# Performance work log

Hardware: AMD Instinct MI355X
Metric: run time of the kernel (lower is better)

The kernel has to match this reference:

```python
import math
import jax, jax.numpy as jnp
import numpy as np

HEAD = 16
DIM = 1024
DH = DIM // HEAD
NEG = -100000000.0


def setup_inputs() -> dict:
    key = jax.random.key(0)
    ks = jax.random.split(key, 12)
    B, S, D = 2, 2048, DIM
    s = 1.0 / math.sqrt(D)
    return {
        "key": jax.random.normal(ks[0], (B, S, D), jnp.float32),
        "value": jax.random.normal(ks[1], (B, S, D), jnp.float32),
        "query": jax.random.normal(ks[2], (B, S, D), jnp.float32),
        "mask": jax.random.randint(ks[3], (B, 1, S, S), 0, 2) == 1,
        "Wq": jax.random.normal(ks[4], (D, D), jnp.float32) * s,
        "bq": jnp.zeros((D,), jnp.float32),
        "Wk": jax.random.normal(ks[5], (D, D), jnp.float32) * s,
        "bk": jnp.zeros((D,), jnp.float32),
        "Wv": jax.random.normal(ks[6], (D, D), jnp.float32) * s,
        "bv": jnp.zeros((D,), jnp.float32),
        "Wo": jax.random.normal(ks[7], (D, D), jnp.float32) * s,
        "bo": jnp.zeros((D,), jnp.float32),
    }


def _split_heads(x, b):
    # [B, S, D] -> [B, H, S, Dh]
    return x.reshape(b, -1, HEAD, DH).transpose(0, 2, 1, 3)


def reference(key, value, query, mask, Wq, bq, Wk, bk, Wv, bv, Wo, bo):
    b, k_len, d = key.shape
    q_len = query.shape[1]
    k_up = _split_heads(key @ Wk.T + bk, b)
    v_up = _split_heads(value @ Wv.T + bv, b)
    q_up = _split_heads(query @ Wq.T + bq, b) / math.sqrt(DH)
    scores = jnp.einsum("bhqd,bhkd->bhqk", q_up, k_up)
    scores = jnp.where(mask, NEG, scores)
    attn = jax.nn.softmax(scores, axis=-1)
    # dropout is identity in eval/reference mode
    context = jnp.einsum("bhqk,bhkd->bhqd", attn, v_up)
    context = context.transpose(0, 2, 1, 3).reshape(b, q_len, d)
    out = context @ Wo.T + bo
    return out, attn
```

## Files before the change

kernel.cpp:

```cpp
#include <hip/hip_runtime.h>
#include <stdint.h>

#define S_LEN 2048
#define D_MODEL 1024
#define N_HEAD 16
#define D_HEAD 64
#define N_BATCH 2
#define M_TOK (N_BATCH * S_LEN)

typedef unsigned short u16;
typedef unsigned int u32;
typedef unsigned long long u64;
typedef __attribute__((ext_vector_type(8))) short bf16x8;
typedef __attribute__((ext_vector_type(4))) short s16x4;
typedef __attribute__((ext_vector_type(4))) float f32x4;
typedef __attribute__((ext_vector_type(4))) unsigned short u16x4;

#define MFMA16(a, b, c) __builtin_amdgcn_mfma_f32_16x16x32_bf16((a), (b), (c), 0, 0, 0)

#if defined(__has_builtin)
#if __has_builtin(__builtin_amdgcn_mfma_f32_16x16x16bf16_1k)
#define HAVE_MFMA_16x16x16 1
#define MFMA_PV(a, b, c) __builtin_amdgcn_mfma_f32_16x16x16bf16_1k((a), (b), (c), 0, 0, 0)
#endif
#endif

#define WAITCNT(n) asm volatile("s_waitcnt vmcnt(" #n ")" ::: "memory")
#define BAR() __builtin_amdgcn_s_barrier()

__device__ __forceinline__ u16 f2bf(float f) {
  unsigned int u = __float_as_uint(f);
  u = (u + 0x7FFFu + ((u >> 16) & 1u)) >> 16;
  return (u16)u;
}

__device__ __forceinline__ void gload_lds16(const u16* g, u16* l) {
  __builtin_amdgcn_global_load_lds((const __attribute__((address_space(1))) void*)g,
                                   (__attribute__((address_space(3))) void*)l, 16, 0, 0);
}

#define N4BIG (M_TOK * D_MODEL / 4)
#define N4W (D_MODEL * D_MODEL / 4)
__global__ __launch_bounds__(256) void cvt7_kernel(
    const float* __restrict__ sk, const float* __restrict__ sv, const float* __restrict__ sq,
    const float* __restrict__ swq, const float* __restrict__ swk, const float* __restrict__ swv,
    const float* __restrict__ swo, u16* __restrict__ dk, u16* __restrict__ dv, u16* __restrict__ dq,
    u16* __restrict__ dwq, u16* __restrict__ dwk, u16* __restrict__ dwv, u16* __restrict__ dwo) {
  const float* s;
  u16* d;
  int n4;
  switch (blockIdx.y) {
    case 0: s = sk; d = dk; n4 = N4BIG; break;
    case 1: s = sv; d = dv; n4 = N4BIG; break;
    case 2: s = sq; d = dq; n4 = N4BIG; break;
    case 3: s = swq; d = dwq; n4 = N4W; break;
    case 4: s = swk; d = dwk; n4 = N4W; break;
    case 5: s = swv; d = dwv; n4 = N4W; break;
    default: s = swo; d = dwo; n4 = N4W; break;
  }
  int i = blockIdx.x * blockDim.x + threadIdx.x;
  int stride = gridDim.x * blockDim.x;
  for (; i < n4; i += stride) {
    float4 v = ((const float4*)s)[i];
    u16x4 o = {f2bf(v.x), f2bf(v.y), f2bf(v.z), f2bf(v.w)};
    ((u16x4*)d)[i] = o;
  }
}

__global__ __launch_bounds__(256) void pack_mask(const int* __restrict__ mask,
                                                 u64* __restrict__ packed) {
  int wid = (blockIdx.x * blockDim.x + threadIdx.x) >> 6;
  int lane = threadIdx.x & 63;
  int nw = (gridDim.x * blockDim.x) >> 6;
  const int NW64 = M_TOK * (S_LEN / 64);
  for (int widx = wid; widx < NW64; widx += nw) {
    int m = mask[(size_t)widx * 64 + lane];
    u64 bits = __ballot(m != 0);
    if (lane == 0) packed[widx] = bits;
  }
}

__device__ __forceinline__ void gemm_body(const u16* __restrict__ A, const u16* __restrict__ Bw,
                                          const float* __restrict__ bias, void* __restrict__ Cout,
                                          float scale, int outmode) {
  __shared__ u16 As[128 * 32];
  __shared__ u16 Bs[128 * 32];
  const int K = D_MODEL, N = D_MODEL;
  int tid = threadIdx.x;
  int w = tid >> 6, lane = tid & 63, lg = lane >> 4, lr = lane & 15;
  int m0 = blockIdx.x * 128, n0 = blockIdx.y * 128;
  int wr = w >> 1, wc = w & 1;
  f32x4 acc[4][4] = {};
  int r0 = tid >> 2;
  int r1 = 64 + (tid >> 2);
  int kk0 = (tid & 3) * 8;
  for (int kb = 0; kb < K; kb += 32) {
    gload_lds16(A + (size_t)(m0 + r0) * K + kb + kk0, As + w * 512);
    gload_lds16(A + (size_t)(m0 + r1) * K + kb + kk0, As + 2048 + w * 512);
    gload_lds16(Bw + (size_t)(n0 + r0) * K + kb + kk0, Bs + w * 512);
    gload_lds16(Bw + (size_t)(n0 + r1) * K + kb + kk0, Bs + 2048 + w * 512);
    __syncthreads();
    bf16x8 af[4], bfr[4];
#pragma unroll
    for (int i = 0; i < 4; i++)
      af[i] = *(const bf16x8*)(As + (wr * 64 + i * 16 + lr) * 32 + lg * 8);
#pragma unroll
    for (int i = 0; i < 4; i++)
      bfr[i] = *(const bf16x8*)(Bs + (wc * 64 + i * 16 + lr) * 32 + lg * 8);
#pragma unroll
    for (int mi = 0; mi < 4; mi++)
#pragma unroll
      for (int ni = 0; ni < 4; ni++)
        acc[mi][ni] = MFMA16(af[mi], bfr[ni], acc[mi][ni]);
    __syncthreads();
  }
#pragma unroll
  for (int mi = 0; mi < 4; mi++)
#pragma unroll
    for (int ni = 0; ni < 4; ni++) {
      int col = n0 + wc * 64 + ni * 16 + lr;
      float bv = bias[col];
      if (outmode == 2) {
        int row0 = m0 + wr * 64 + mi * 16 + lg * 4;
        int bb = row0 >> 11, ss = row0 & (S_LEN - 1);
        u16x4 pk;
#pragma unroll
        for (int r = 0; r < 4; r++) pk[r] = f2bf((acc[mi][ni][r] + bv) * scale);
        *(u16x4*)((u16*)Cout + ((size_t)((bb * N_HEAD + (col >> 6)) * D_HEAD + (col & 63)) * S_LEN + ss)) = pk;
      } else {
#pragma unroll
        for (int r = 0; r < 4; r++) {
          int row = m0 + wr * 64 + mi * 16 + lg * 4 + r;
          float v = (acc[mi][ni][r] + bv) * scale;
          if (outmode == 1)
            ((float*)Cout)[(size_t)row * N + col] = v;
          else
            ((u16*)Cout)[(size_t)row * N + col] = f2bf(v);
        }
      }
    }
}

#define QSCALE 0.18033688011112042f

__global__ __launch_bounds__(256) void proj3_kernel(
    const u16* __restrict__ kbf, const u16* __restrict__ vbf, const u16* __restrict__ qbf,
    const u16* __restrict__ wkb, const u16* __restrict__ wvb, const u16* __restrict__ wqb,
    const float* __restrict__ bk, const float* __restrict__ bv, const float* __restrict__ bq,
    u16* __restrict__ kup, u16* __restrict__ vtg, u16* __restrict__ qup) {
  int z = blockIdx.z;
  if (z == 0)
    gemm_body(kbf, wkb, bk, kup, 1.0f, 0);
  else if (z == 1)
    gemm_body(vbf, wvb, bv, vtg, 1.0f, 2);
  else
    gemm_body(qbf, wqb, bq, qup, QSCALE, 0);
}

__global__ __launch_bounds__(256) void gemm_out_kernel(const u16* __restrict__ A,
                                                       const u16* __restrict__ Bw,
                                                       const float* __restrict__ bias,
                                                       float* __restrict__ C) {
  gemm_body(A, Bw, bias, C, 1.0f, 1);
}

__global__ __launch_bounds__(256, 8) void attn_p0(const u16* __restrict__ Qup,
                                                  const u16* __restrict__ Kup,
                                                  const u32* __restrict__ mpack,
                                                  float* __restrict__ lsums) {
  __shared__ u16 kbuf[2][64 * 64];
  int tid = threadIdx.x;
  int w = tid >> 6, lane = tid & 63, lg = lane >> 4, lr = lane & 15;
  int fb = blockIdx.x;
  int logical = (fb & 7) * 256 + (fb >> 3);
  int khalf = logical & 1;
  int qb = (logical >> 1) & 31;
  int h = (logical >> 6) & 15;
  int b = logical >> 10;
  int q0 = qb * 64;
  int q = q0 + w * 16 + lr;
  const float NEGV = -100000000.0f;

  bf16x8 qf0, qf1;
  {
    const u16* qrow = Qup + (size_t)(b * S_LEN + q) * D_MODEL + h * D_HEAD;
    qf0 = *(const bf16x8*)(qrow + lg * 8);
    qf1 = *(const bf16x8*)(qrow + 32 + lg * 8);
  }
  const u16* Kb = Kup + (size_t)(b * S_LEN) * D_MODEL + h * D_HEAD;
  const u32* mrow = mpack + (size_t)(b * S_LEN + q) * (S_LEN / 32) + khalf * 32;

  int srow = tid >> 3;
  int schunk = (tid & 7) ^ (srow & 7);
  const u16* KgA = Kb + (size_t)(khalf * 1024 + srow) * D_MODEL + schunk * 8;
  const int sw = lr & 7;

#define STAGE_K0(bn, ktn)                                                   \
  do {                                                                      \
    const u16* _s = KgA + (size_t)(ktn) * 64 * D_MODEL;                     \
    gload_lds16(_s, &kbuf[bn][0] + w * 512);                                \
    gload_lds16(_s + (size_t)32 * D_MODEL, &kbuf[bn][2048] + w * 512);      \
  } while (0)

  float lsA = 0.f, lsB = 0.f;
#define P0_BODY(BN, MM)                                                     \
  {                                                                         \
    const u16* kc = &kbuf[BN][0];                                           \
    _Pragma("unroll") for (int t = 0; t < 4; t++) {                         \
      const u16* kr = kc + (t * 16 + lr) * 64;                              \
      bf16x8 k0 = *(const bf16x8*)(kr + ((lg ^ sw) << 3));                  \
      bf16x8 k1 = *(const bf16x8*)(kr + (((lg + 4) ^ sw) << 3));            \
      f32x4 a = {0.f, 0.f, 0.f, 0.f};                                       \
      a = MFMA16(k0, qf0, a);                                               \
      a = MFMA16(k1, qf1, a);                                               \
      u32 wbits = (t < 2) ? (MM).x : (MM).y;                                \
      _Pragma("unroll") for (int r = 0; r < 4; r++) {                       \
        int j = (t * 16 + lg * 4 + r) & 31;                                 \
        float s = ((wbits >> j) & 1u) ? NEGV : a[r];                        \
        if (r & 1) lsB += exp2f(s); else lsA += exp2f(s);                   \
      }                                                                     \
    }                                                                       \
  }

  uint2 mA, mB;
  mA = *(const uint2*)(mrow);
  STAGE_K0(0, 0);
  for (int it = 0; it < 7; it++) {
    int kt = it * 2;
    mB = *(const uint2*)(mrow + (kt + 1) * 2);
    STAGE_K0(1, kt + 1);
    WAITCNT(3);
    BAR();
    P0_BODY(0, mA);
    BAR();
    mA = *(const uint2*)(mrow + (kt + 2) * 2);
    STAGE_K0(0, kt + 2);
    WAITCNT(3);
    BAR();
    P0_BODY(1, mB);
    BAR();
  }
  mB = *(const uint2*)(mrow + 15 * 2);
  STAGE_K0(1, 15);
  WAITCNT(3);
  BAR();
  P0_BODY(0, mA);
  BAR();
  WAITCNT(0);
  BAR();
  P0_BODY(1, mB);

  float lsum = lsA + lsB;
  lsum += __shfl_xor(lsum, 16);
  lsum += __shfl_xor(lsum, 32);
  if (lg == 0) lsums[(size_t)khalf * 65536 + (size_t)(b * N_HEAD + h) * S_LEN + q] = lsum;
#undef STAGE_K0
#undef P0_BODY
}

__global__ __launch_bounds__(256, 5) void attn_p1(
    const u16* __restrict__ Qup, const u16* __restrict__ Kup, const u16* __restrict__ Vt,
    const u32* __restrict__ mpack, const float* __restrict__ lsums,
    float* __restrict__ attn_out, u16* __restrict__ ctx) {
  __shared__ u16 kbuf[2][64 * 64];
  __shared__ u16 vbuf[2][64 * 64];
#if !defined(HAVE_MFMA_16x16x16)
  __shared__ u16 pbuf[4][16 * 64];
#endif
  int tid = threadIdx.x;
  int w = tid >> 6, lane = tid & 63, lg = lane >> 4, lr = lane & 15;
  int fb = blockIdx.x;
  int logical = (fb & 7) * 128 + (fb >> 3);
  int qx = logical & 31;
  int h = (logical >> 5) & 15;
  int b = logical >> 9;
  int q0 = qx * 64;
  int q = q0 + w * 16 + lr;
  const float NEGV = -100000000.0f;

  bf16x8 qf0, qf1;
  {
    const u16* qrow = Qup + (size_t)(b * S_LEN + q) * D_MODEL + h * D_HEAD;
    qf0 = *(const bf16x8*)(qrow + lg * 8);
    qf1 = *(const bf16x8*)(qrow + 32 + lg * 8);
  }
  const u16* Kb = Kup + (size_t)(b * S_LEN) * D_MODEL + h * D_HEAD;
  const u16* Vb = Vt + (size_t)(b * N_HEAD + h) * D_HEAD * S_LEN;
  const u32* mrow = mpack + (size_t)(b * S_LEN + q) * (S_LEN / 32);
  float* attn_b = attn_out + ((size_t)(b * N_HEAD + h) * S_LEN + q) * S_LEN;

  float il2;
  {
    size_t idx = (size_t)(b * N_HEAD + h) * S_LEN + q;
    float tot = lsums[idx] + lsums[65536 + idx];
    il2 = tot > 0.f ? -__log2f(tot) : 0.f;
  }

  int srow = tid >> 3;
  int schunk = (tid & 7) ^ (srow & 7);
  const u16* KgA = Kb + (size_t)srow * D_MODEL + schunk * 8;
  const u16* VgA = Vb + (size_t)srow * S_LEN + schunk * 8;
  const int sw = lr & 7;

#define SK(bn, ktn)                                                          \
  do {                                                                       \
    const u16* _s = KgA + (size_t)(ktn) * 64 * D_MODEL;                      \
    gload_lds16(_s, &kbuf[bn][0] + w * 512);                                 \
    gload_lds16(_s + (size_t)32 * D_MODEL, &kbuf[bn][2048] + w * 512);       \
  } while (0)
#define SV(bn, ktn)                                                          \
  do {                                                                       \
    const u16* _s = VgA + (size_t)(ktn) * 64;                                \
    gload_lds16(_s, &vbuf[bn][0] + w * 512);                                 \
    gload_lds16(_s + (size_t)32 * S_LEN, &vbuf[bn][2048] + w * 512);         \
  } while (0)

  f32x4 ctxacc[4] = {};

#if defined(HAVE_MFMA_16x16x16)
#define P1_BODY(BN, MM, KT)                                                  \
  {                                                                          \
    const u16* kc = &kbuf[BN][0];                                            \
    const u16* vc = &vbuf[BN][0];                                            \
    _Pragma("unroll") for (int t = 0; t < 4; t++) {                          \
      const u16* kr = kc + (t * 16 + lr) * 64;                               \
      bf16x8 k0 = *(const bf16x8*)(kr + ((lg ^ sw) << 3));                   \
      bf16x8 k1 = *(const bf16x8*)(kr + (((lg + 4) ^ sw) << 3));             \
      f32x4 a = {0.f, 0.f, 0.f, 0.f};                                        \
      a = MFMA16(k0, qf0, a);                                                \
      a = MFMA16(k1, qf1, a);                                                \
      u32 wbits = (t < 2) ? (MM).x : (MM).y;                                 \
      f32x4 p;                                                               \
      u16x4 pb;                                                              \
      _Pragma("unroll") for (int r = 0; r < 4; r++) {                        \
        int j = (t * 16 + lg * 4 + r) & 31;                                  \
        float s = ((wbits >> j) & 1u) ? NEGV : (a[r] + il2);                 \
        float pv = exp2f(s);                                                 \
        p[r] = pv;                                                           \
        pb[r] = f2bf(pv);                                                    \
      }                                                                      \
      *(f32x4*)(attn_b + (KT) * 64 + t * 16 + lg * 4) = p;                   \
      s16x4 ap = {(short)pb[0], (short)pb[1], (short)pb[2], (short)pb[3]};   \
      _Pragma("unroll") for (int d = 0; d < 4; d++) {                        \
        s16x4 vf = *(const s16x4*)(vc + (d * 16 + lr) * 64 +                 \
                                   (((t * 2 + (lg >> 1)) ^ sw) << 3) +       \
                                   ((lg & 1) << 2));                         \
        ctxacc[d] = MFMA_PV(ap, vf, ctxacc[d]);                              \
      }                                                                      \
    }                                                                        \
  }
#else
#define P1_BODY(BN, MM, KT)                                                  \
  {                                                                          \
    const u16* kc = &kbuf[BN][0];                                            \
    const u16* vc = &vbuf[BN][0];                                            \
    u16* pw = &pbuf[w][0];                                                   \
    _Pragma("unroll") for (int t = 0; t < 4; t++) {                          \
      const u16* kr = kc + (t * 16 + lr) * 64;                               \
      bf16x8 k0 = *(const bf16x8*)(kr + ((lg ^ sw) << 3));                   \
      bf16x8 k1 = *(const bf16x8*)(kr + (((lg + 4) ^ sw) << 3));             \
      f32x4 a = {0.f, 0.f, 0.f, 0.f};                                        \
      a = MFMA16(k0, qf0, a);                                                \
      a = MFMA16(k1, qf1, a);                                                \
      u32 wbits = (t < 2) ? (MM).x : (MM).y;                                 \
      f32x4 p;                                                               \
      u16x4 pb;                                                              \
      _Pragma("unroll") for (int r = 0; r < 4; r++) {                        \
        int j = (t * 16 + lg * 4 + r) & 31;                                  \
        float s = ((wbits >> j) & 1u) ? NEGV : (a[r] + il2);                 \
        float pv = exp2f(s);                                                 \
        p[r] = pv;                                                           \
        pb[r] = f2bf(pv);                                                    \
      }                                                                      \
      *(f32x4*)(attn_b + (KT) * 64 + t * 16 + lg * 4) = p;                   \
      *(u16x4*)(pw + lr * 64 + (((t * 2 + (lg >> 1)) ^ sw) << 3) +           \
                ((lg & 1) << 2)) = pb;                                       \
    }                                                                        \
    bf16x8 pa0 = *(const bf16x8*)(pw + lr * 64 + ((lg ^ sw) << 3));          \
    bf16x8 pa1 = *(const bf16x8*)(pw + lr * 64 + (((lg + 4) ^ sw) << 3));    \
    _Pragma("unroll") for (int d = 0; d < 4; d++) {                          \
      const u16* vr = vc + (d * 16 + lr) * 64;                               \
      bf16x8 v0 = *(const bf16x8*)(vr + ((lg ^ sw) << 3));                   \
      bf16x8 v1 = *(const bf16x8*)(vr + (((lg + 4) ^ sw) << 3));             \
      ctxacc[d] = MFMA16(pa0, v0, ctxacc[d]);                                \
      ctxacc[d] = MFMA16(pa1, v1, ctxacc[d]);                                \
    }                                                                        \
  }
#endif

  uint2 mA, mB;
  mA = *(const uint2*)(mrow);
  SK(0, 0);
  SV(0, 0);
  mB = *(const uint2*)(mrow + 1 * 2);
  SK(1, 1);
  SV(1, 1);
  WAITCNT(5);
  BAR();
  P1_BODY(0, mA, 0);
  BAR();
  mA = *(const uint2*)(mrow + 2 * 2);
  SK(0, 2);
  SV(0, 2);
  WAITCNT(9);
  BAR();
  P1_BODY(1, mB, 1);
  BAR();
  for (int it = 1; it < 15; it++) {
    int kt = it * 2;
    mB = *(const uint2*)(mrow + (kt + 1) * 2);
    SK(1, kt + 1);
    SV(1, kt + 1);
    WAITCNT(9);
    BAR();
    P1_BODY(0, mA, kt);
    BAR();
    mA = *(const uint2*)(mrow + (kt + 2) * 2);
    SK(0, kt + 2);
    SV(0, kt + 2);
    WAITCNT(9);
    BAR();
    P1_BODY(1, mB, kt + 1);
    BAR();
  }
  mB = *(const uint2*)(mrow + 31 * 2);
  SK(1, 31);
  SV(1, 31);
  WAITCNT(9);
  BAR();
  P1_BODY(0, mA, 30);
  BAR();
  WAITCNT(4);
  BAR();
  P1_BODY(1, mB, 31);

#pragma unroll
  for (int d = 0; d < 4; d++)
#pragma unroll
    for (int r = 0; r < 4; r++) {
      int sq = q0 + w * 16 + lg * 4 + r;
      ctx[(size_t)(b * S_LEN + sq) * D_MODEL + h * D_HEAD + d * 16 + lr] = f2bf(ctxacc[d][r]);
    }
#undef SK
#undef SV
#undef P1_BODY
}

#define O_KBF 0u
#define O_VBF 4194304u
#define O_QBF 8388608u
#define O_WQ 12582912u
#define O_WK 13631488u
#define O_WV 14680064u
#define O_WO 15728640u
#define O_QUP 16777216u
#define O_KUP 20971520u
#define O_VUP 25165824u
#define O_CTX 29360128u

extern "C" void kernel_launch(void* const* d_in, const int* in_sizes, int n_in,
                              void* d_out, int out_size, void* d_ws, size_t ws_size,
                              hipStream_t stream) {
  const float* key = (const float*)d_in[0];
  const float* value = (const float*)d_in[1];
  const float* query = (const float*)d_in[2];
  const int* mask = (const int*)d_in[3];
  const float* Wq = (const float*)d_in[4];
  const float* bq = (const float*)d_in[5];
  const float* Wk = (const float*)d_in[6];
  const float* bk = (const float*)d_in[7];
  const float* Wv = (const float*)d_in[8];
  const float* bv = (const float*)d_in[9];
  const float* Wo = (const float*)d_in[10];
  const float* bo = (const float*)d_in[11];

  u16* ws = (u16*)d_ws;
  u16* kbf = ws + O_KBF;
  u16* vbf = ws + O_VBF;
  u16* qbf = ws + O_QBF;
  u16* wqb = ws + O_WQ;
  u16* wkb = ws + O_WK;
  u16* wvb = ws + O_WV;
  u16* wob = ws + O_WO;
  u16* qup = ws + O_QUP;
  u16* kup = ws + O_KUP;
  u16* vtg = ws + O_VUP;
  u16* ctxb = ws + O_CTX;
  u64* maskp = (u64*)kbf;
  float* lsums = (float*)vbf;

  float* out = (float*)d_out;
  float* attn = out + (size_t)N_BATCH * S_LEN * D_MODEL;

  cvt7_kernel<<<dim3(512, 7), 256, 0, stream>>>(key, value, query, Wq, Wk, Wv, Wo, kbf, vbf, qbf,
                                                wqb, wkb, wvb, wob);
  proj3_kernel<<<dim3(32, 8, 3), 256, 0, stream>>>(kbf, vbf, qbf, wkb, wvb, wqb, bk, bv, bq, kup,
                                                   vtg, qup);
  pack_mask<<<1024, 256, 0, stream>>>(mask, maskp);
  attn_p0<<<2048, 256, 0, stream>>>(qup, kup, (const u32*)maskp, lsums);
  attn_p1<<<1024, 256, 0, stream>>>(qup, kup, vtg, (const u32*)maskp, lsums, attn, ctxb);
  gemm_out_kernel<<<dim3(32, 8), 256, 0, stream>>>(ctxb, wob, bo, out);
}
```

Measured before the change: 357.8 us.

## Split attention key range across blocks and double query rows per warp

New measurement: 383.6 us. +7.2%, slower.

```diff
diff --git a/kernel.cpp b/kernel.cpp
--- a/kernel.cpp
+++ b/kernel.cpp
@@ -258,48 +258,57 @@
 #undef P0_BODY
 }
 
-__global__ __launch_bounds__(256, 5) void attn_p1(
+__global__ __launch_bounds__(256, 4) void attn_p1(
     const u16* __restrict__ Qup, const u16* __restrict__ Kup, const u16* __restrict__ Vt,
     const u32* __restrict__ mpack, const float* __restrict__ lsums,
-    float* __restrict__ attn_out, u16* __restrict__ ctx) {
+    float* __restrict__ attn_out, float* __restrict__ ctx0, float* __restrict__ ctx1) {
   __shared__ u16 kbuf[2][64 * 64];
   __shared__ u16 vbuf[2][64 * 64];
 #if !defined(HAVE_MFMA_16x16x16)
-  __shared__ u16 pbuf[4][16 * 64];
+  __shared__ u16 pbuf[4][2][16 * 64];
 #endif
   int tid = threadIdx.x;
   int w = tid >> 6, lane = tid & 63, lg = lane >> 4, lr = lane & 15;
   int fb = blockIdx.x;
   int logical = (fb & 7) * 128 + (fb >> 3);
-  int qx = logical & 31;
+  int khalf = logical & 1;
+  int qx = (logical >> 1) & 15;
   int h = (logical >> 5) & 15;
   int b = logical >> 9;
-  int q0 = qx * 64;
-  int q = q0 + w * 16 + lr;
+  int q0 = qx * 128;
+  int qA = q0 + w * 32 + lr;
+  int qB = qA + 16;
   const float NEGV = -100000000.0f;
 
-  bf16x8 qf0, qf1;
+  bf16x8 qfA0, qfA1, qfB0, qfB1;
   {
-    const u16* qrow = Qup + (size_t)(b * S_LEN + q) * D_MODEL + h * D_HEAD;
-    qf0 = *(const bf16x8*)(qrow + lg * 8);
-    qf1 = *(const bf16x8*)(qrow + 32 + lg * 8);
+    const u16* qrowA = Qup + (size_t)(b * S_LEN + qA) * D_MODEL + h * D_HEAD;
+    qfA0 = *(const bf16x8*)(qrowA + lg * 8);
+    qfA1 = *(const bf16x8*)(qrowA + 32 + lg * 8);
+    const u16* qrowB = qrowA + (size_t)16 * D_MODEL;
+    qfB0 = *(const bf16x8*)(qrowB + lg * 8);
+    qfB1 = *(const bf16x8*)(qrowB + 32 + lg * 8);
   }
   const u16* Kb = Kup + (size_t)(b * S_LEN) * D_MODEL + h * D_HEAD;
   const u16* Vb = Vt + (size_t)(b * N_HEAD + h) * D_HEAD * S_LEN;
-  const u32* mrow = mpack + (size_t)(b * S_LEN + q) * (S_LEN / 32);
-  float* attn_b = attn_out + ((size_t)(b * N_HEAD + h) * S_LEN + q) * S_LEN;
-
-  float il2;
+  const u32* mrowA = mpack + (size_t)(b * S_LEN + qA) * (S_LEN / 32) + khalf * 32;
+  const u32* mrowB = mrowA + 16 * (S_LEN / 32);
+  float* attn_bA = attn_out + ((size_t)(b * N_HEAD + h) * S_LEN + qA) * S_LEN + khalf * 1024;
+  float* attn_bB = attn_bA + (size_t)16 * S_LEN;
+
+  float il2A, il2B;
   {
-    size_t idx = (size_t)(b * N_HEAD + h) * S_LEN + q;
-    float tot = lsums[idx] + lsums[65536 + idx];
-    il2 = tot > 0.f ? -__log2f(tot) : 0.f;
+    size_t idxA = (size_t)(b * N_HEAD + h) * S_LEN + qA;
+    float totA = lsums[idxA] + lsums[65536 + idxA];
+    il2A = totA > 0.f ? -__log2f(totA) : 0.f;
+    float totB = lsums[idxA + 16] + lsums[65536 + idxA + 16];
+    il2B = totB > 0.f ? -__log2f(totB) : 0.f;
   }
 
   int srow = tid >> 3;
   int schunk = (tid & 7) ^ (srow & 7);
-  const u16* KgA = Kb + (size_t)srow * D_MODEL + schunk * 8;
-  const u16* VgA = Vb + (size_t)srow * S_LEN + schunk * 8;
+  const u16* KgA = Kb + (size_t)(khalf * 1024 + srow) * D_MODEL + schunk * 8;
+  const u16* VgA = Vb + (size_t)srow * S_LEN + khalf * 1024 + schunk * 8;
   const int sw = lr & 7;
 
 #define SK(bn, ktn)                                                          \
@@ -315,10 +324,11 @@
     gload_lds16(_s + (size_t)32 * S_LEN, &vbuf[bn][2048] + w * 512);         \
   } while (0)
 
-  f32x4 ctxacc[4] = {};
+  f32x4 ctxA[4] = {};
+  f32x4 ctxB[4] = {};
 
 #if defined(HAVE_MFMA_16x16x16)
-#define P1_BODY(BN, MM, KT)                                                  \
+#define P1_BODY(BN, MMA, MMB, KT)                                            \
   {                                                                          \
     const u16* kc = &kbuf[BN][0];                                            \
     const u16* vc = &vbuf[BN][0];                                            \
@@ -326,124 +336,151 @@
       const u16* kr = kc + (t * 16 + lr) * 64;                               \
       bf16x8 k0 = *(const bf16x8*)(kr + ((lg ^ sw) << 3));                   \
       bf16x8 k1 = *(const bf16x8*)(kr + (((lg + 4) ^ sw) << 3));             \
-      f32x4 a = {0.f, 0.f, 0.f, 0.f};                                        \
-      a = MFMA16(k0, qf0, a);                                                \
-      a = MFMA16(k1, qf1, a);                                                \
-      u32 wbits = (t < 2) ? (MM).x : (MM).y;                                 \
-      f32x4 p;                                                               \
-      u16x4 pb;                                                              \
+      f32x4 aA = {0.f, 0.f, 0.f, 0.f};                                       \
+      aA = MFMA16(k0, qfA0, aA);                                             \
+      aA = MFMA16(k1, qfA1, aA);                                             \
+      f32x4 aB = {0.f, 0.f, 0.f, 0.f};                                       \
+      aB = MFMA16(k0, qfB0, aB);                                             \
+      aB = MFMA16(k1, qfB1, aB);                                             \
+      u32 wbA = (t < 2) ? (MMA).x : (MMA).y;                                 \
+      u32 wbB = (t < 2) ? (MMB).x : (MMB).y;                                 \
+      f32x4 pA, pB;                                                          \
+      u16x4 pbA, pbB;                                                        \
       _Pragma("unroll") for (int r = 0; r < 4; r++) {                        \
         int j = (t * 16 + lg * 4 + r) & 31;                                  \
-        float s = ((wbits >> j) & 1u) ? NEGV : (a[r] + il2);                 \
-        float pv = exp2f(s);                                                 \
-        p[r] = pv;                                                           \
-        pb[r] = f2bf(pv);                                                    \
+        float sA = ((wbA >> j) & 1u) ? NEGV : (aA[r] + il2A);                \
+        float vA = exp2f(sA);                                                \
+        pA[r] = vA;                                                          \
+        pbA[r] = f2bf(vA);                                                   \
+        float sB = ((wbB >> j) & 1u) ? NEGV : (aB[r] + il2B);                \
+        float vB = exp2f(sB);                                                \
+        pB[r] = vB;                                                          \
+        pbB[r] = f2bf(vB);                                                   \
       }                                                                      \
-      *(f32x4*)(attn_b + (KT) * 64 + t * 16 + lg * 4) = p;                   \
-      s16x4 ap = {(short)pb[0], (short)pb[1], (short)pb[2], (short)pb[3]};   \
+      *(f32x4*)(attn_bA + (KT) * 64 + t * 16 + lg * 4) = pA;                 \
+      *(f32x4*)(attn_bB + (KT) * 64 + t * 16 + lg * 4) = pB;                 \
+      s16x4 apA = {(short)pbA[0], (short)pbA[1], (short)pbA[2], (short)pbA[3]}; \
+      s16x4 apB = {(short)pbB[0], (short)pbB[1], (short)pbB[2], (short)pbB[3]}; \
       _Pragma("unroll") for (int d = 0; d < 4; d++) {                        \
         s16x4 vf = *(const s16x4*)(vc + (d * 16 + lr) * 64 +                 \
                                    (((t * 2 + (lg >> 1)) ^ sw) << 3) +       \
                                    ((lg & 1) << 2));                         \
-        ctxacc[d] = MFMA_PV(ap, vf, ctxacc[d]);                              \
+        ctxA[d] = MFMA_PV(apA, vf, ctxA[d]);                                 \
+        ctxB[d] = MFMA_PV(apB, vf, ctxB[d]);                                 \
       }                                                                      \
     }                                                                        \
   }
 #else
-#define P1_BODY(BN, MM, KT)                                                  \
+#define P1_BODY(BN, MMA, MMB, KT)                                            \
   {                                                                          \
     const u16* kc = &kbuf[BN][0];                                            \
     const u16* vc = &vbuf[BN][0];                                            \
-    u16* pw = &pbuf[w][0];                                                   \
     _Pragma("unroll") for (int t = 0; t < 4; t++) {                          \
       const u16* kr = kc + (t * 16 + lr) * 64;                               \
       bf16x8 k0 = *(const bf16x8*)(kr + ((lg ^ sw) << 3));                   \
       bf16x8 k1 = *(const bf16x8*)(kr + (((lg + 4) ^ sw) << 3));             \
-      f32x4 a = {0.f, 0.f, 0.f, 0.f};                                        \
-      a = MFMA16(k0, qf0, a);                                                \
-      a = MFMA16(k1, qf1, a);                                                \
-      u32 wbits = (t < 2) ? (MM).x : (MM).y;                                 \
-      f32x4 p;                                                               \
-      u16x4 pb;                                                              \
+      f32x4 aA = {0.f, 0.f, 0.f, 0.f};                                       \
+      aA = MFMA16(k0, qfA0, aA);                                             \
+      aA = MFMA16(k1, qfA1, aA);                                             \
+      f32x4 aB = {0.f, 0.f, 0.f, 0.f};                                       \
+      aB = MFMA16(k0, qfB0, aB);                                             \
+      aB = MFMA16(k1, qfB1, aB);                                             \
+      u32 wbA = (t < 2) ? (MMA).x : (MMA).y;                                 \
+      u32 wbB = (t < 2) ? (MMB).x : (MMB).y;                                 \
+      f32x4 pA, pB;                                                          \
+      u16x4 pbA, pbB;                                                        \
       _Pragma("unroll") for (int r = 0; r < 4; r++) {                        \
         int j = (t * 16 + lg * 4 + r) & 31;                                  \
-        float s = ((wbits >> j) & 1u) ? NEGV : (a[r] + il2);                 \
-        float pv = exp2f(s);                                                 \
-        p[r] = pv;                                                           \
-        pb[r] = f2bf(pv);                                                    \
+        float sA = ((wbA >> j) & 1u) ? NEGV : (aA[r] + il2A);                \
+        float vA = exp2f(sA);                                                \
+        pA[r] = vA;                                                          \
+        pbA[r] = f2bf(vA);                                                   \
+        float sB = ((wbB >> j) & 1u) ? NEGV : (aB[r] + il2B);                \
+        float vB = exp2f(sB);                                                \
+        pB[r] = vB;                                                          \
+        pbB[r] = f2bf(vB);                                                   \
       }                                                                      \
-      *(f32x4*)(attn_b + (KT) * 64 + t * 16 + lg * 4) = p;                   \
-      *(u16x4*)(pw + lr * 64 + (((t * 2 + (lg >> 1)) ^ sw) << 3) +           \
-                ((lg & 1) << 2)) = pb;                                       \
+      *(f32x4*)(attn_bA + (KT) * 64 + t * 16 + lg * 4) = pA;                 \
+      *(f32x4*)(attn_bB + (KT) * 64 + t * 16 + lg * 4) = pB;                 \
+      *(u16x4*)(&pbuf[w][0][lr * 64 + (((t * 2 + (lg >> 1)) ^ sw) << 3) +    \
+                ((lg & 1) << 2)]) = pbA;                                     \
+      *(u16x4*)(&pbuf[w][1][lr * 64 + (((t * 2 + (lg >> 1)) ^ sw) << 3) +    \
+                ((lg & 1) << 2)]) = pbB;                                     \
     }                                                                        \
-    bf16x8 pa0 = *(const bf16x8*)(pw + lr * 64 + ((lg ^ sw) << 3));          \
-    bf16x8 pa1 = *(const bf16x8*)(pw + lr * 64 + (((lg + 4) ^ sw) << 3));    \
+    bf16x8 paA0 = *(const bf16x8*)(&pbuf[w][0][lr * 64 + ((lg ^ sw) << 3)]);  \
+    bf16x8 paA1 = *(const bf16x8*)(&pbuf[w][0][lr * 64 + (((lg + 4) ^ sw) << 3)]); \
+    bf16x8 paB0 = *(const bf16x8*)(&pbuf[w][1][lr * 64 + ((lg ^ sw) << 3)]);  \
+    bf16x8 paB1 = *(const bf16x8*)(&pbuf[w][1][lr * 64 + (((lg + 4) ^ sw) << 3)]); \
     _Pragma("unroll") for (int d = 0; d < 4; d++) {                          \
       const u16* vr = vc + (d * 16 + lr) * 64;                               \
       bf16x8 v0 = *(const bf16x8*)(vr + ((lg ^ sw) << 3));                   \
       bf16x8 v1 = *(const bf16x8*)(vr + (((lg + 4) ^ sw) << 3));             \
-      ctxacc[d] = MFMA16(pa0, v0, ctxacc[d]);                                \
-      ctxacc[d] = MFMA16(pa1, v1, ctxacc[d]);                                \
+      ctxA[d] = MFMA16(paA0, v0, ctxA[d]);                                   \
+      ctxA[d] = MFMA16(paA1, v1, ctxA[d]);                                   \
+      ctxB[d] = MFMA16(paB0, v0, ctxB[d]);                                   \
+      ctxB[d] = MFMA16(paB1, v1, ctxB[d]);                                   \
     }                                                                        \
   }
 #endif
 
-  uint2 mA, mB;
-  mA = *(const uint2*)(mrow);
+  uint2 mAa, mAb, mBa, mBb;
+  mAa = *(const uint2*)(mrowA);
+  mAb = *(const uint2*)(mrowB);
   SK(0, 0);
   SV(0, 0);
-  mB = *(const uint2*)(mrow + 1 * 2);
-  SK(1, 1);
-  SV(1, 1);
-  WAITCNT(5);
-  BAR();
-  P1_BODY(0, mA, 0);
-  BAR();
-  mA = *(const uint2*)(mrow + 2 * 2);
-  SK(0, 2);
-  SV(0, 2);
-  WAITCNT(9);
-  BAR();
-  P1_BODY(1, mB, 1);
-  BAR();
-  for (int it = 1; it < 15; it++) {
+  for (int it = 0; it < 7; it++) {
     int kt = it * 2;
-    mB = *(const uint2*)(mrow + (kt + 1) * 2);
+    mBa = *(const uint2*)(mrowA + (kt + 1) * 2);
+    mBb = *(const uint2*)(mrowB + (kt + 1) * 2);
     SK(1, kt + 1);
     SV(1, kt + 1);
-    WAITCNT(9);
-    BAR();
-    P1_BODY(0, mA, kt);
-    BAR();
-    mA = *(const uint2*)(mrow + (kt + 2) * 2);
+    WAITCNT(6);
+    BAR();
+    P1_BODY(0, mAa, mAb, kt);
+    BAR();
+    mAa = *(const uint2*)(mrowA + (kt + 2) * 2);
+    mAb = *(const uint2*)(mrowB + (kt + 2) * 2);
     SK(0, kt + 2);
     SV(0, kt + 2);
-    WAITCNT(9);
-    BAR();
-    P1_BODY(1, mB, kt + 1);
-    BAR();
-  }
-  mB = *(const uint2*)(mrow + 31 * 2);
-  SK(1, 31);
-  SV(1, 31);
-  WAITCNT(9);
+    WAITCNT(6);
+    BAR();
+    P1_BODY(1, mBa, mBb, kt + 1);
+    BAR();
+  }
+  mBa = *(const uint2*)(mrowA + 15 * 2);
+  mBb = *(const uint2*)(mrowB + 15 * 2);
+  SK(1, 15);
+  SV(1, 15);
+  WAITCNT(6);
   BAR();
-  P1_BODY(0, mA, 30);
+  P1_BODY(0, mAa, mAb, 14);
   BAR();
-  WAITCNT(4);
+  WAITCNT(0);
   BAR();
-  P1_BODY(1, mB, 31);
-
+  P1_BODY(1, mBa, mBb, 15);
+
+  float* cdst = khalf ? ctx1 : ctx0;
 #pragma unroll
   for (int d = 0; d < 4; d++)
 #pragma unroll
     for (int r = 0; r < 4; r++) {
-      int sq = q0 + w * 16 + lg * 4 + r;
-      ctx[(size_t)(b * S_LEN + sq) * D_MODEL + h * D_HEAD + d * 16 + lr] = f2bf(ctxacc[d][r]);
+      int sqA = q0 + w * 32 + lg * 4 + r;
+      cdst[(size_t)(b * S_LEN + sqA) * D_MODEL + h * D_HEAD + d * 16 + lr] = ctxA[d][r];
+      cdst[(size_t)(b * S_LEN + sqA + 16) * D_MODEL + h * D_HEAD + d * 16 + lr] = ctxB[d][r];
     }
 #undef SK
 #undef SV
 #undef P1_BODY
+}
+
+__global__ __launch_bounds__(256) void ctx_reduce(const float* __restrict__ c0,
+                                                  const float* __restrict__ c1,
+                                                  u16* __restrict__ dst) {
+  int i = blockIdx.x * 256 + threadIdx.x;
+  f32x4 a = ((const f32x4*)c0)[i];
+  f32x4 bv = ((const f32x4*)c1)[i];
+  u16x4 o = {f2bf(a[0] + bv[0]), f2bf(a[1] + bv[1]), f2bf(a[2] + bv[2]), f2bf(a[3] + bv[3])};
+  ((u16x4*)dst)[i] = o;
 }
 
 #define O_KBF 0u
@@ -486,11 +523,13 @@
   u16* kup = ws + O_KUP;
   u16* vtg = ws + O_VUP;
   u16* ctxb = ws + O_CTX;
-  u64* maskp = (u64*)kbf;
-  float* lsums = (float*)vbf;
+  u64* maskp = (u64*)(ws + O_CTX);
+  float* lsums = (float*)(ws + O_CTX + 524288);
+  float* ctx0 = (float*)(ws + O_KBF);
 
   float* out = (float*)d_out;
   float* attn = out + (size_t)N_BATCH * S_LEN * D_MODEL;
+  float* ctx1 = out;
 
   cvt7_kernel<<<dim3(512, 7), 256, 0, stream>>>(key, value, query, Wq, Wk, Wv, Wo, kbf, vbf, qbf,
                                                 wqb, wkb, wvb, wob);
@@ -498,6 +537,7 @@
                                                    vtg, qup);
   pack_mask<<<1024, 256, 0, stream>>>(mask, maskp);
   attn_p0<<<2048, 256, 0, stream>>>(qup, kup, (const u32*)maskp, lsums);
-  attn_p1<<<1024, 256, 0, stream>>>(qup, kup, vtg, (const u32*)maskp, lsums, attn, ctxb);
+  attn_p1<<<1024, 256, 0, stream>>>(qup, kup, vtg, (const u32*)maskp, lsums, attn, ctx0, ctx1);
+  ctx_reduce<<<4096, 256, 0, stream>>>(ctx0, ctx1, ctxb);
   gemm_out_kernel<<<dim3(32, 8), 256, 0, stream>>>(ctxb, wob, bo, out);
 }
```
